# Optimization experiments

Hardware: AMD Instinct MI355X
Metric: run time of the kernel (lower is better)

## Reference

```python
import jax, jax.numpy as jnp
import numpy as np

N_NODES = 100000
N_EDGES = 800000
FEATURE_DIM = 128
DEPTH = 3


def setup_inputs() -> dict:
    key = jax.random.key(0)
    k1, k2, k3 = jax.random.split(key, 3)
    x = jax.random.normal(k1, (N_NODES, FEATURE_DIM), dtype=jnp.float32)
    edge_index = jax.random.randint(k2, (2, N_EDGES), 0, N_NODES, dtype=jnp.int32)
    W = jax.random.normal(k3, (FEATURE_DIM, FEATURE_DIM), dtype=jnp.float32) * (1.0 / np.sqrt(FEATURE_DIM))
    b = jnp.zeros((FEATURE_DIM,), dtype=jnp.float32)
    return {"x": x, "edge_index": edge_index, "W": W, "b": b}


def reference(x, edge_index, W, b):
    n = x.shape[0]
    # PyG GCNConv default: add self-loops, symmetric normalization
    loop = jnp.arange(n, dtype=edge_index.dtype)
    src = jnp.concatenate([edge_index[0], loop])  # [E+N]
    dst = jnp.concatenate([edge_index[1], loop])  # [E+N]
    ones = jnp.ones(src.shape[0], dtype=x.dtype)
    deg = jax.ops.segment_sum(ones, dst, num_segments=n)  # in-degree incl. self-loop
    dis = jnp.where(deg > 0, jax.lax.rsqrt(deg), 0.0)  # deg^{-1/2}
    norm = (dis[src] * dis[dst])[:, None]  # [E+N, 1]

    # depth iterations share the SAME conv weights (time-invariant)
    for _ in range(DEPTH):
        h = x @ W  # [N, D] linear transform first (PyG order)
        msg = h[src] * norm  # gather + normalize, [E+N, D]
        agg = jax.ops.segment_sum(msg, dst, num_segments=n)  # scatter-add
        x = jax.nn.relu(agg + b)  # bias, NullControl adds 0, dropout_rate=0 is identity
    return x
```

## Files before the change

### kernel.cpp

```cpp
#include <hip/hip_runtime.h>

#define FD 128

typedef __attribute__((ext_vector_type(8))) short short8;
typedef __attribute__((ext_vector_type(4))) float floatx4;

__device__ inline unsigned short f2bf(float f) {
  unsigned u = __float_as_uint(f);
  u += 0x7fffu + ((u >> 16) & 1u);
  return (unsigned short)(u >> 16);
}
__device__ inline float bf2f(unsigned short s) {
  return __uint_as_float(((unsigned)s) << 16);
}


__global__ __launch_bounds__(256) void k_count(const int* __restrict__ dst,
                                               int* __restrict__ deg, int E) {
  int e = blockIdx.x * 256 + threadIdx.x;
  if (e < E) atomicAdd(&deg[dst[e]], 1);
}

__global__ __launch_bounds__(256) void k_dis(const int* __restrict__ deg,
                                             float* __restrict__ dis, int N) {
  int i = blockIdx.x * 256 + threadIdx.x;
  if (i < N) dis[i] = rsqrtf((float)(deg[i] + 1));
}

__global__ __launch_bounds__(256) void k_scanA(const int* __restrict__ deg,
                                               int* __restrict__ offtmp,
                                               int* __restrict__ bsum, int N) {
  __shared__ int s[256];
  int i = blockIdx.x * 256 + threadIdx.x;
  int v = (i < N) ? deg[i] : 0;
  s[threadIdx.x] = v;
  __syncthreads();
#pragma unroll
  for (int ofs = 1; ofs < 256; ofs <<= 1) {
    int t = (threadIdx.x >= ofs) ? s[threadIdx.x - ofs] : 0;
    __syncthreads();
    s[threadIdx.x] += t;
    __syncthreads();
  }
  if (i < N) offtmp[i] = s[threadIdx.x] - v;
  if (threadIdx.x == 255) bsum[blockIdx.x] = s[255];
}

__global__ __launch_bounds__(512) void k_scanB(int* __restrict__ bsum, int nb) {
  __shared__ int s[512];
  int t = threadIdx.x;
  int v = (t < nb) ? bsum[t] : 0;
  s[t] = v;
  __syncthreads();
#pragma unroll
  for (int ofs = 1; ofs < 512; ofs <<= 1) {
    int u = (t >= ofs) ? s[t - ofs] : 0;
    __syncthreads();
    s[t] += u;
    __syncthreads();
  }
  if (t < nb) bsum[t] = s[t] - v;
}

__global__ __launch_bounds__(256) void k_scanC(const int* __restrict__ offtmp,
                                               const int* __restrict__ bsum,
                                               int* __restrict__ off, int N, int E) {
  int i = blockIdx.x * 256 + threadIdx.x;
  if (i < N) off[i] = offtmp[i] + bsum[i >> 8];
  if (i == 0) off[N] = E;
}

__global__ __launch_bounds__(256) void k_fill(const int* __restrict__ src,
                                              const int* __restrict__ dst,
                                              const float* __restrict__ dis,
                                              const int* __restrict__ off,
                                              int* __restrict__ cursor,
                                              int2* __restrict__ ew, int E) {
  int e = blockIdx.x * 256 + threadIdx.x;
  if (e >= E) return;
  int d = dst[e], s = src[e];
  int pos = off[d] + atomicAdd(&cursor[d], 1);
  ew[pos] = make_int2(s, __float_as_int(dis[s] * dis[d]));
}

__global__ __launch_bounds__(256) void k_wsplit(const float* __restrict__ W,
                                                short* __restrict__ hi,
                                                short* __restrict__ lo) {
  int idx = blockIdx.x * 256 + threadIdx.x;
  int j = idx & 7, lane = (idx >> 3) & 63, kt = (idx >> 9) & 3, ct = idx >> 11;
  int k = kt * 32 + (lane >> 4) * 8 + j;
  int n = ct * 16 + (lane & 15);
  float w = W[k * FD + n];
  unsigned short h = f2bf(w);
  hi[idx] = (short)h;
  lo[idx] = (short)f2bf(w - bf2f(h));
}

template <bool ABF16>
__global__ __launch_bounds__(256) void k_gemm(const void* __restrict__ Av,
                                              const short* __restrict__ Wf_hi,
                                              const short* __restrict__ Wf_lo,
                                              unsigned short* __restrict__ H, int N) {
  __shared__ short whi[FD * FD], wlo[FD * FD];
  int tid = threadIdx.x;
#pragma unroll
  for (int it = 0; it < 8; ++it) {
    int idx = (it * 256 + tid) * 8;
    *(short8*)&whi[idx] = *(const short8*)&Wf_hi[idx];
    *(short8*)&wlo[idx] = *(const short8*)&Wf_lo[idx];
  }
  __syncthreads();

  int wid = tid >> 6, lane = tid & 63;
  int quad = lane >> 4, m = lane & 15;
  int rbase = blockIdx.x * 128 + wid * 32;

  short8 ahi[2][4], alo[2][4];
#pragma unroll
  for (int t = 0; t < 2; ++t) {
    int arow = rbase + t * 16 + m;
    if (arow >= N) arow = N - 1;
    if (ABF16) {
      const unsigned short* ap = (const unsigned short*)Av + (size_t)arow * FD;
#pragma unroll
      for (int kt = 0; kt < 4; ++kt)
        ahi[t][kt] = *(const short8*)(ap + kt * 32 + quad * 8);
    } else {
      const float* ap = (const float*)Av + (size_t)arow * FD;
#pragma unroll
      for (int kt = 0; kt < 4; ++kt) {
        const float* p = ap + kt * 32 + quad * 8;
        float4 a0 = *(const float4*)p;
        float4 a1 = *(const float4*)(p + 4);
        float av[8] = {a0.x, a0.y, a0.z, a0.w, a1.x, a1.y, a1.z, a1.w};
#pragma unroll
        for (int j = 0; j < 8; ++j) {
          unsigned short hb = f2bf(av[j]);
          ahi[t][kt][j] = (short)hb;
          alo[t][kt][j] = (short)f2bf(av[j] - bf2f(hb));
        }
      }
    }
  }

#pragma unroll
  for (int ct = 0; ct < 8; ++ct) {
    floatx4 acc0 = {0.f, 0.f, 0.f, 0.f}, acc1 = {0.f, 0.f, 0.f, 0.f};
#pragma unroll
    for (int kt = 0; kt < 4; ++kt) {
      int fo = (((ct << 2) + kt) * 64 + lane) * 8;
      short8 bhi = *(const short8*)&whi[fo];
      short8 blo = *(const short8*)&wlo[fo];
      acc0 = __builtin_amdgcn_mfma_f32_16x16x32_bf16(ahi[0][kt], bhi, acc0, 0, 0, 0);
      acc1 = __builtin_amdgcn_mfma_f32_16x16x32_bf16(ahi[1][kt], bhi, acc1, 0, 0, 0);
      if (!ABF16) {
        acc0 = __builtin_amdgcn_mfma_f32_16x16x32_bf16(alo[0][kt], bhi, acc0, 0, 0, 0);
        acc1 = __builtin_amdgcn_mfma_f32_16x16x32_bf16(alo[1][kt], bhi, acc1, 0, 0, 0);
      }
      acc0 = __builtin_amdgcn_mfma_f32_16x16x32_bf16(ahi[0][kt], blo, acc0, 0, 0, 0);
      acc1 = __builtin_amdgcn_mfma_f32_16x16x32_bf16(ahi[1][kt], blo, acc1, 0, 0, 0);
    }
#pragma unroll
    for (int r = 0; r < 4; ++r) {
      int row0 = rbase + quad * 4 + r;
      int row1 = rbase + 16 + quad * 4 + r;
      if (row0 < N) H[(size_t)row0 * FD + ct * 16 + m] = f2bf(acc0[r]);
      if (row1 < N) H[(size_t)row1 * FD + ct * 16 + m] = f2bf(acc1[r]);
    }
  }
}

template <bool OUTBF16>
__global__ __launch_bounds__(256) void k_agg(const unsigned int* __restrict__ h,
                                             const int* __restrict__ off,
                                             const int2* __restrict__ ew,
                                             const float* __restrict__ dis,
                                             const float* __restrict__ bias,
                                             void* __restrict__ out, int N) {
  int wid = __builtin_amdgcn_readfirstlane(threadIdx.x >> 6);
  int lane = threadIdx.x & 63;
  int i = blockIdx.x * 4 + wid;
  if (i >= N) return;
  float di = dis[i];
  float wself = di * di;
  unsigned v = h[(size_t)i * 64 + lane];
  float a0 = wself * __uint_as_float(v << 16);
  float a1 = wself * __uint_as_float(v & 0xffff0000u);
  float b0 = 0.f, b1 = 0.f, c0 = 0.f, c1 = 0.f, d0 = 0.f, d1 = 0.f;
  int p = off[i], p1 = off[i + 1];
  for (; p + 3 < p1; p += 4) {
    int2 e0 = ew[p], e1 = ew[p + 1], e2 = ew[p + 2], e3 = ew[p + 3];
    unsigned v0 = h[(size_t)e0.x * 64 + lane];
    unsigned v1 = h[(size_t)e1.x * 64 + lane];
    unsigned v2 = h[(size_t)e2.x * 64 + lane];
    unsigned v3 = h[(size_t)e3.x * 64 + lane];
    float w0 = __int_as_float(e0.y), w1 = __int_as_float(e1.y);
    float w2 = __int_as_float(e2.y), w3 = __int_as_float(e3.y);
    a0 = fmaf(w0, __uint_as_float(v0 << 16), a0);
    a1 = fmaf(w0, __uint_as_float(v0 & 0xffff0000u), a1);
    b0 = fmaf(w1, __uint_as_float(v1 << 16), b0);
    b1 = fmaf(w1, __uint_as_float(v1 & 0xffff0000u), b1);
    c0 = fmaf(w2, __uint_as_float(v2 << 16), c0);
    c1 = fmaf(w2, __uint_as_float(v2 & 0xffff0000u), c1);
    d0 = fmaf(w3, __uint_as_float(v3 << 16), d0);
    d1 = fmaf(w3, __uint_as_float(v3 & 0xffff0000u), d1);
  }
  for (; p < p1; ++p) {
    int2 e0 = ew[p];
    unsigned v0 = h[(size_t)e0.x * 64 + lane];
    float w0 = __int_as_float(e0.y);
    a0 = fmaf(w0, __uint_as_float(v0 << 16), a0);
    a1 = fmaf(w0, __uint_as_float(v0 & 0xffff0000u), a1);
  }
  float2 bb = ((const float2*)bias)[lane];
  float o0 = fmaxf(a0 + b0 + c0 + d0 + bb.x, 0.f);
  float o1 = fmaxf(a1 + b1 + c1 + d1 + bb.y, 0.f);
  if (OUTBF16) {
    unsigned pk = ((unsigned)f2bf(o1) << 16) | (unsigned)f2bf(o0);
    ((unsigned*)out)[(size_t)i * 64 + lane] = pk;
  } else {
    ((float2*)out)[(size_t)i * 64 + lane] = make_float2(o0, o1);
  }
}


extern "C" void kernel_launch(void* const* d_in, const int* in_sizes, int n_in,
                              void* d_out, int out_size, void* d_ws, size_t ws_size,
                              hipStream_t stream) {
  const float* x = (const float*)d_in[0];
  const int* ei = (const int*)d_in[1];
  const float* Wg = (const float*)d_in[2];
  const float* b = (const float*)d_in[3];
  int N = in_sizes[0] / FD;
  int E = in_sizes[1] / 2;
  const int* src = ei;
  const int* dst = ei + E;

  char* p = (char*)d_ws;
  auto alloc = [&](size_t bytes) {
    void* r = (void*)p;
    p += (bytes + 255) & ~(size_t)255;
    return r;
  };
  int* deg = (int*)alloc((size_t)N * 4);
  int* cursor = (int*)alloc((size_t)N * 4);
  float* dis = (float*)alloc((size_t)N * 4);
  int* offtmp = (int*)alloc((size_t)N * 4);
  int nb = (N + 255) / 256;
  int* bsum = (int*)alloc((size_t)nb * 4);
  int* off = (int*)alloc((size_t)(N + 1) * 4);
  int2* ew = (int2*)alloc((size_t)E * 8);
  unsigned short* h = (unsigned short*)alloc((size_t)N * FD * 2);
  unsigned short* xb = (unsigned short*)alloc((size_t)N * FD * 2);
  short* wf_hi = (short*)alloc((size_t)FD * FD * 2);
  short* wf_lo = (short*)alloc((size_t)FD * FD * 2);

  hipMemsetAsync(deg, 0, (size_t)N * 4, stream);
  hipMemsetAsync(cursor, 0, (size_t)N * 4, stream);

  int gE = (E + 255) / 256, gN = (N + 255) / 256;
  k_count<<<gE, 256, 0, stream>>>(dst, deg, E);
  k_dis<<<gN, 256, 0, stream>>>(deg, dis, N);
  k_scanA<<<nb, 256, 0, stream>>>(deg, offtmp, bsum, N);
  k_scanB<<<1, 512, 0, stream>>>(bsum, nb);
  k_scanC<<<gN, 256, 0, stream>>>(offtmp, bsum, off, N, E);
  k_fill<<<gE, 256, 0, stream>>>(src, dst, dis, off, cursor, ew, E);
  k_wsplit<<<FD * FD / 256, 256, 0, stream>>>(Wg, wf_hi, wf_lo);

  int gG = (N + 127) / 128;
  int gA = (N + 3) / 4;
  k_gemm<false><<<gG, 256, 0, stream>>>(x, wf_hi, wf_lo, h, N);
  k_agg<true><<<gA, 256, 0, stream>>>((const unsigned*)h, off, ew, dis, b, xb, N);
  k_gemm<true><<<gG, 256, 0, stream>>>(xb, wf_hi, wf_lo, h, N);
  k_agg<true><<<gA, 256, 0, stream>>>((const unsigned*)h, off, ew, dis, b, xb, N);
  k_gemm<true><<<gG, 256, 0, stream>>>(xb, wf_hi, wf_lo, h, N);
  k_agg<false><<<gA, 256, 0, stream>>>((const unsigned*)h, off, ew, dis, b, d_out, N);
}
```

Measured before the change: 361.4 us.

## Process four nodes per wave in aggregation with software-pipelined gathers, drop W-lo for bf16 layers

The aggregation kernel now assigns four consecutive destination nodes to each wavefront and walks their combined CSR edge range as one stream. Edge records and feature rows are prefetched two stages ahead to hide gather latency, and each edge is routed to the right node's accumulator. The later GEMMs skip the low-part W correction, which halves their MFMA work and LDS use but lowers accuracy. The separate k_dis kernel is folded into scanA, removing one launch.

```diff
diff --git a/kernel.cpp b/kernel.cpp
--- a/kernel.cpp
+++ b/kernel.cpp
@@ -13,6 +13,9 @@
 __device__ inline float bf2f(unsigned short s) {
   return __uint_as_float(((unsigned)s) << 16);
 }
+__device__ inline float lo16f(unsigned v) { return __uint_as_float(v << 16); }
+__device__ inline float hi16f(unsigned v) { return __uint_as_float(v & 0xffff0000u); }
+__device__ inline int imin(int a, int b) { return a < b ? a : b; }
 
 
 __global__ __launch_bounds__(256) void k_count(const int* __restrict__ dst,
@@ -21,18 +24,14 @@
   if (e < E) atomicAdd(&deg[dst[e]], 1);
 }
 
-__global__ __launch_bounds__(256) void k_dis(const int* __restrict__ deg,
-                                             float* __restrict__ dis, int N) {
-  int i = blockIdx.x * 256 + threadIdx.x;
-  if (i < N) dis[i] = rsqrtf((float)(deg[i] + 1));
-}
-
 __global__ __launch_bounds__(256) void k_scanA(const int* __restrict__ deg,
                                                int* __restrict__ offtmp,
-                                               int* __restrict__ bsum, int N) {
+                                               int* __restrict__ bsum,
+                                               float* __restrict__ dis, int N) {
   __shared__ int s[256];
   int i = blockIdx.x * 256 + threadIdx.x;
   int v = (i < N) ? deg[i] : 0;
+  if (i < N) dis[i] = rsqrtf((float)(v + 1));
   s[threadIdx.x] = v;
   __syncthreads();
 #pragma unroll
@@ -96,18 +95,19 @@
   lo[idx] = (short)f2bf(w - bf2f(h));
 }
 
-template <bool ABF16>
+template <bool ABF16, bool WLO>
 __global__ __launch_bounds__(256) void k_gemm(const void* __restrict__ Av,
                                               const short* __restrict__ Wf_hi,
                                               const short* __restrict__ Wf_lo,
                                               unsigned short* __restrict__ H, int N) {
-  __shared__ short whi[FD * FD], wlo[FD * FD];
+  __shared__ short whi[FD * FD];
+  __shared__ short wlo[WLO ? FD * FD : 8];
   int tid = threadIdx.x;
 #pragma unroll
   for (int it = 0; it < 8; ++it) {
     int idx = (it * 256 + tid) * 8;
     *(short8*)&whi[idx] = *(const short8*)&Wf_hi[idx];
-    *(short8*)&wlo[idx] = *(const short8*)&Wf_lo[idx];
+    if (WLO) *(short8*)&wlo[idx] = *(const short8*)&Wf_lo[idx];
   }
   __syncthreads();
 
@@ -150,15 +150,17 @@
     for (int kt = 0; kt < 4; ++kt) {
       int fo = (((ct << 2) + kt) * 64 + lane) * 8;
       short8 bhi = *(const short8*)&whi[fo];
-      short8 blo = *(const short8*)&wlo[fo];
       acc0 = __builtin_amdgcn_mfma_f32_16x16x32_bf16(ahi[0][kt], bhi, acc0, 0, 0, 0);
       acc1 = __builtin_amdgcn_mfma_f32_16x16x32_bf16(ahi[1][kt], bhi, acc1, 0, 0, 0);
       if (!ABF16) {
         acc0 = __builtin_amdgcn_mfma_f32_16x16x32_bf16(alo[0][kt], bhi, acc0, 0, 0, 0);
         acc1 = __builtin_amdgcn_mfma_f32_16x16x32_bf16(alo[1][kt], bhi, acc1, 0, 0, 0);
       }
-      acc0 = __builtin_amdgcn_mfma_f32_16x16x32_bf16(ahi[0][kt], blo, acc0, 0, 0, 0);
-      acc1 = __builtin_amdgcn_mfma_f32_16x16x32_bf16(ahi[1][kt], blo, acc1, 0, 0, 0);
+      if (WLO) {
+        short8 blo = *(const short8*)&wlo[fo];
+        acc0 = __builtin_amdgcn_mfma_f32_16x16x32_bf16(ahi[0][kt], blo, acc0, 0, 0, 0);
+        acc1 = __builtin_amdgcn_mfma_f32_16x16x32_bf16(ahi[1][kt], blo, acc1, 0, 0, 0);
+      }
     }
 #pragma unroll
     for (int r = 0; r < 4; ++r) {
@@ -177,49 +179,86 @@
                                              const float* __restrict__ dis,
                                              const float* __restrict__ bias,
                                              void* __restrict__ out, int N) {
-  int wid = __builtin_amdgcn_readfirstlane(threadIdx.x >> 6);
   int lane = threadIdx.x & 63;
-  int i = blockIdx.x * 4 + wid;
-  if (i >= N) return;
-  float di = dis[i];
-  float wself = di * di;
-  unsigned v = h[(size_t)i * 64 + lane];
-  float a0 = wself * __uint_as_float(v << 16);
-  float a1 = wself * __uint_as_float(v & 0xffff0000u);
-  float b0 = 0.f, b1 = 0.f, c0 = 0.f, c1 = 0.f, d0 = 0.f, d1 = 0.f;
-  int p = off[i], p1 = off[i + 1];
-  for (; p + 3 < p1; p += 4) {
-    int2 e0 = ew[p], e1 = ew[p + 1], e2 = ew[p + 2], e3 = ew[p + 3];
-    unsigned v0 = h[(size_t)e0.x * 64 + lane];
-    unsigned v1 = h[(size_t)e1.x * 64 + lane];
-    unsigned v2 = h[(size_t)e2.x * 64 + lane];
-    unsigned v3 = h[(size_t)e3.x * 64 + lane];
-    float w0 = __int_as_float(e0.y), w1 = __int_as_float(e1.y);
-    float w2 = __int_as_float(e2.y), w3 = __int_as_float(e3.y);
-    a0 = fmaf(w0, __uint_as_float(v0 << 16), a0);
-    a1 = fmaf(w0, __uint_as_float(v0 & 0xffff0000u), a1);
-    b0 = fmaf(w1, __uint_as_float(v1 << 16), b0);
-    b1 = fmaf(w1, __uint_as_float(v1 & 0xffff0000u), b1);
-    c0 = fmaf(w2, __uint_as_float(v2 << 16), c0);
-    c1 = fmaf(w2, __uint_as_float(v2 & 0xffff0000u), c1);
-    d0 = fmaf(w3, __uint_as_float(v3 << 16), d0);
-    d1 = fmaf(w3, __uint_as_float(v3 & 0xffff0000u), d1);
-  }
-  for (; p < p1; ++p) {
-    int2 e0 = ew[p];
-    unsigned v0 = h[(size_t)e0.x * 64 + lane];
-    float w0 = __int_as_float(e0.y);
-    a0 = fmaf(w0, __uint_as_float(v0 << 16), a0);
-    a1 = fmaf(w0, __uint_as_float(v0 & 0xffff0000u), a1);
-  }
+  int i0 = __builtin_amdgcn_readfirstlane((blockIdx.x * 4 + (threadIdx.x >> 6)) * 4);
+  if (i0 >= N) return;
+
+  int b0 = off[i0];
+  int b1 = off[imin(i0 + 1, N)];
+  int b2 = off[imin(i0 + 2, N)];
+  int b3 = off[imin(i0 + 3, N)];
+  int b4 = off[imin(i0 + 4, N)];
+
+  float ax[4], ay[4];
+#pragma unroll
+  for (int t = 0; t < 4; ++t) {
+    int i = i0 + t;
+    if (i < N) {
+      float di = dis[i];
+      float ws = di * di;
+      unsigned v = h[(size_t)i * 64 + lane];
+      ax[t] = ws * lo16f(v);
+      ay[t] = ws * hi16f(v);
+    } else {
+      ax[t] = 0.f;
+      ay[t] = 0.f;
+    }
+  }
+
+  int p = b0, pe = b4;
+  if (p < pe) {
+    int2 e0[4], e1[4];
+    unsigned g0[4];
+#pragma unroll
+    for (int j = 0; j < 4; ++j) e0[j] = ew[imin(p + j, pe - 1)];
+#pragma unroll
+    for (int j = 0; j < 4; ++j) g0[j] = h[(size_t)e0[j].x * 64 + lane];
+#pragma unroll
+    for (int j = 0; j < 4; ++j) e1[j] = ew[imin(p + 4 + j, pe - 1)];
+
+    for (int q = p; q < pe; q += 4) {
+      unsigned g1[4];
+      int2 e2[4];
+#pragma unroll
+      for (int j = 0; j < 4; ++j) g1[j] = h[(size_t)e1[j].x * 64 + lane];
+#pragma unroll
+      for (int j = 0; j < 4; ++j) e2[j] = ew[imin(q + 8 + j, pe - 1)];
+#pragma unroll
+      for (int j = 0; j < 4; ++j) {
+        int qq = q + j;
+        if (qq < pe) {
+          float w = __int_as_float(e0[j].y);
+          float l = lo16f(g0[j]), hh = hi16f(g0[j]);
+          if (qq < b1) {
+            ax[0] = fmaf(w, l, ax[0]); ay[0] = fmaf(w, hh, ay[0]);
+          } else if (qq < b2) {
+            ax[1] = fmaf(w, l, ax[1]); ay[1] = fmaf(w, hh, ay[1]);
+          } else if (qq < b3) {
+            ax[2] = fmaf(w, l, ax[2]); ay[2] = fmaf(w, hh, ay[2]);
+          } else {
+            ax[3] = fmaf(w, l, ax[3]); ay[3] = fmaf(w, hh, ay[3]);
+          }
+        }
+      }
+#pragma unroll
+      for (int j = 0; j < 4; ++j) { e0[j] = e1[j]; e1[j] = e2[j]; g0[j] = g1[j]; }
+    }
+  }
+
   float2 bb = ((const float2*)bias)[lane];
-  float o0 = fmaxf(a0 + b0 + c0 + d0 + bb.x, 0.f);
-  float o1 = fmaxf(a1 + b1 + c1 + d1 + bb.y, 0.f);
-  if (OUTBF16) {
-    unsigned pk = ((unsigned)f2bf(o1) << 16) | (unsigned)f2bf(o0);
-    ((unsigned*)out)[(size_t)i * 64 + lane] = pk;
-  } else {
-    ((float2*)out)[(size_t)i * 64 + lane] = make_float2(o0, o1);
+#pragma unroll
+  for (int t = 0; t < 4; ++t) {
+    int i = i0 + t;
+    if (i < N) {
+      float o0 = fmaxf(ax[t] + bb.x, 0.f);
+      float o1 = fmaxf(ay[t] + bb.y, 0.f);
+      if (OUTBF16) {
+        unsigned pk = ((unsigned)f2bf(o1) << 16) | (unsigned)f2bf(o0);
+        ((unsigned*)out)[(size_t)i * 64 + lane] = pk;
+      } else {
+        ((float2*)out)[(size_t)i * 64 + lane] = make_float2(o0, o1);
+      }
+    }
   }
 }
 
@@ -260,19 +299,18 @@
 
   int gE = (E + 255) / 256, gN = (N + 255) / 256;
   k_count<<<gE, 256, 0, stream>>>(dst, deg, E);
-  k_dis<<<gN, 256, 0, stream>>>(deg, dis, N);
-  k_scanA<<<nb, 256, 0, stream>>>(deg, offtmp, bsum, N);
+  k_scanA<<<nb, 256, 0, stream>>>(deg, offtmp, bsum, dis, N);
   k_scanB<<<1, 512, 0, stream>>>(bsum, nb);
   k_scanC<<<gN, 256, 0, stream>>>(offtmp, bsum, off, N, E);
   k_fill<<<gE, 256, 0, stream>>>(src, dst, dis, off, cursor, ew, E);
   k_wsplit<<<FD * FD / 256, 256, 0, stream>>>(Wg, wf_hi, wf_lo);
 
   int gG = (N + 127) / 128;
-  int gA = (N + 3) / 4;
-  k_gemm<false><<<gG, 256, 0, stream>>>(x, wf_hi, wf_lo, h, N);
+  int gA = (N + 15) / 16;
+  k_gemm<false, true><<<gG, 256, 0, stream>>>(x, wf_hi, wf_lo, h, N);
   k_agg<true><<<gA, 256, 0, stream>>>((const unsigned*)h, off, ew, dis, b, xb, N);
-  k_gemm<true><<<gG, 256, 0, stream>>>(xb, wf_hi, wf_lo, h, N);
+  k_gemm<true, false><<<gG, 256, 0, stream>>>(xb, wf_hi, wf_lo, h, N);
   k_agg<true><<<gA, 256, 0, stream>>>((const unsigned*)h, off, ew, dis, b, xb, N);
-  k_gemm<true><<<gG, 256, 0, stream>>>(xb, wf_hi, wf_lo, h, N);
+  k_gemm<true, false><<<gG, 256, 0, stream>>>(xb, wf_hi, wf_lo, h, N);
   k_agg<false><<<gA, 256, 0, stream>>>((const unsigned*)h, off, ew, dis, b, d_out, N);
 }
```

New measurement: 361.8 us. About the same (+0.1%).
